# Optimization experiments

Hardware: AMD Instinct MI355X
Metric: run time of the kernel (lower is better)

The kernel has to match this reference:

```python
import jax, jax.numpy as jnp
import numpy as np

B, K, NP = 2, 48, 25            # batch, context_length, grid_x*grid_y
C, H, L = 768, 12, 6            # n_embd, n_head, n_layer
COLORS, VOCAB, IS = 10, 40, 26  # color_num, vocab_size, intention_size
MAXT = 1000                     # max_timestep
TOK = NP + 4                    # tokens per timestep (rtg, 25 states, action, pnp, intention)
T = K * TOK                     # total sequence length


def layernorm(x, g, b, eps=1e-5):
    m = x.mean(-1, keepdims=True)
    v = ((x - m) ** 2).mean(-1, keepdims=True)
    return (x - m) * jax.lax.rsqrt(v + eps) * g + b


def causal_attn(x, wq, bq, wk, bk, wv, bv, wo, bo):
    Bx, Tx, Cx = x.shape
    hd = Cx // H
    def heads(w, bb):
        return (x @ w + bb).reshape(Bx, Tx, H, hd).transpose(0, 2, 1, 3)
    q, k, v = heads(wq, bq), heads(wk, bk), heads(wv, bv)
    att = jnp.einsum('bhqd,bhkd->bhqk', q, k) * (1.0 / np.sqrt(hd))
    mask = jnp.tril(jnp.ones((Tx, Tx), bool))
    att = jnp.where(mask, att, -jnp.inf)
    att = jax.nn.softmax(att, axis=-1)
    y = jnp.einsum('bhqk,bhkd->bhqd', att, v).transpose(0, 2, 1, 3).reshape(Bx, Tx, Cx)
    return y @ wo + bo


def setup_inputs() -> dict:
    key = jax.random.key(0)
    ks = iter(jax.random.split(key, 64))
    def nrm(shape):
        return jax.random.normal(next(ks), shape, jnp.float32) * 0.02
    inp = dict(
        states=jax.random.randint(next(ks), (B, K * NP), 0, COLORS),
        actions=jax.random.randint(next(ks), (B, K), 0, VOCAB),
        rtgs=jax.random.normal(next(ks), (B, K), jnp.float32),
        timesteps=jax.random.randint(next(ks), (B, K), 0, MAXT + 1),
        pnp=jax.random.normal(next(ks), (B, K, NP), jnp.float32),
        intentions=jax.random.randint(next(ks), (B, K, 2), 0, IS),
        pos_emb=nrm((K + 1, C)),               # (block_size, C)
        global_pos_emb=nrm((MAXT + 1, C)),
        state_tab=nrm((COLORS, C)),
        action_tab=nrm((VOCAB, C)),
        ret_W=nrm((1, C)), ret_b=jnp.zeros((C,)),
        pnp_W=nrm((NP, C)), pnp_b=jnp.zeros((C,)),
        src_tab=nrm((IS, C)), dst_tab=nrm((IS, C)),
        int_W=nrm((2 * C, C)), int_b=jnp.zeros((C,)),
        ln1_g=jnp.ones((L, C)), ln1_b=jnp.zeros((L, C)),
        ln2_g=jnp.ones((L, C)), ln2_b=jnp.zeros((L, C)),
        Wq=nrm((L, C, C)), bq=jnp.zeros((L, C)),
        Wk=nrm((L, C, C)), bk=jnp.zeros((L, C)),
        Wv=nrm((L, C, C)), bv=jnp.zeros((L, C)),
        Wo=nrm((L, C, C)), bo=jnp.zeros((L, C)),
        Wm1=nrm((L, C, 4 * C)), bm1=jnp.zeros((L, 4 * C)),
        Wm2=nrm((L, 4 * C, C)), bm2=jnp.zeros((L, C)),
        lnf_g=jnp.ones((C,)), lnf_b=jnp.zeros((C,)),
        Whs=nrm((C, COLORS)), bhs=jnp.zeros((COLORS,)),
        Wha=nrm((C, VOCAB)), bha=jnp.zeros((VOCAB,)),
        Whr=nrm((C, 1)), bhr=jnp.zeros((1,)),
        Whi=nrm((C, 2 * IS)), bhi=jnp.zeros((2 * IS,)),
    )
    return inp


def reference(states, actions, rtgs, timesteps, pnp, intentions,
              pos_emb, global_pos_emb, state_tab, action_tab,
              ret_W, ret_b, pnp_W, pnp_b, src_tab, dst_tab, int_W, int_b,
              ln1_g, ln1_b, ln2_g, ln2_b, Wq, bq, Wk, bk, Wv, bv, Wo, bo,
              Wm1, bm1, Wm2, bm2, lnf_g, lnf_b,
              Whs, bhs, Wha, bha, Whr, bhr, Whi, bhi):
    # --- embeddings, interleaved as [rtg, state_0..24, action, pnp, intention] per timestep ---
    st = state_tab[states].reshape(B, K, NP, C)                    # strided writes 1+i::TOK
    ae = action_tab[actions][:, :, None, :]
    re = (rtgs[..., None] @ ret_W + ret_b)[:, :, None, :]          # rtgs.unsqueeze(-1) -> Linear(1,C)
    pe = (pnp @ pnp_W + pnp_b)[:, :, None, :]
    ie_in = jnp.concatenate([src_tab[intentions[..., 0]], dst_tab[intentions[..., 1]]], axis=-1)
    ie = (ie_in @ int_W + int_b)[:, :, None, :]
    tok = jnp.concatenate([re, st, ae, pe, ie], axis=2).reshape(B, T, C)
    # --- positions: gather global + local pos_emb[:block_size-1], repeat_interleave by TOK ---
    pos = global_pos_emb[timesteps] + pos_emb[:K][None]            # (B, K, C)
    x = tok + jnp.repeat(pos, TOK, axis=1)
    # --- transformer stack (dropout p=0) ---
    def blk(h, p):
        l1g, l1b, l2g, l2b, wq, bq_, wk, bk_, wv, bv_, wo, bo_, w1, b1, w2, b2 = p
        h = h + causal_attn(layernorm(h, l1g, l1b), wq, bq_, wk, bk_, wv, bv_, wo, bo_)
        m = layernorm(h, l2g, l2b)
        h = h + jax.nn.gelu(m @ w1 + b1, approximate=False) @ w2 + b2
        return h, None
    x, _ = jax.lax.scan(blk, x, (ln1_g, ln1_b, ln2_g, ln2_b, Wq, bq, Wk, bk, Wv, bv, Wo, bo, Wm1, bm1, Wm2, bm2))
    x = layernorm(x, lnf_g, lnf_b)
    xr = x.reshape(B, K, TOK, C)
    logits = x @ Whs + bhs                                         # (B, T, COLORS)
    logit_action = xr[:, :, NP + 1] @ Wha + bha                    # (B, K, VOCAB)
    logit_rtg = (xr[:, :, 0] @ Whr + bhr)[..., 0]                  # (B, K)
    li = xr[:, :, NP + 3] @ Whi + bhi                              # (B, K, 2*IS)
    return logits, logit_action, logit_rtg, li[..., :IS], li[..., IS:]
```

## Files before the change

kernel.cpp:

```cpp
#include <hip/hip_runtime.h>
#include <hip/hip_bf16.h>
#include <math.h>


typedef __hip_bfloat16 bf16;
typedef __attribute__((ext_vector_type(4))) short s4v;
typedef __attribute__((ext_vector_type(8))) short s8v;
typedef __attribute__((ext_vector_type(4))) float f4v;
typedef unsigned int u32;

#define DEV static __device__ __forceinline__

constexpr int NBATCH = 2;
constexpr int NK   = 48;
constexpr int NNP  = 25;
constexpr int NC   = 768;
constexpr int NH   = 12;
constexpr int NL   = 6;
constexpr int NTOK = 29;
constexpr int NT   = NK * NTOK;
constexpr int NM   = NBATCH * NT;
constexpr int MPAD = 2816;

DEV float bs2f(short s) {
  unsigned u = ((unsigned)(unsigned short)s) << 16;
  float f; __builtin_memcpy(&f, &u, 4); return f;
}
DEV short f2bs(float f) {
  bf16 h = __float2bfloat16(f);
  short s; __builtin_memcpy(&s, &h, 2); return s;
}

DEV void async16(const short* g, short* l) {
  __builtin_amdgcn_global_load_lds(
      (const __attribute__((address_space(1))) u32*)g,
      (__attribute__((address_space(3))) u32*)l, 16, 0, 0);
}

__global__ __launch_bounds__(256) void transpose_kernel(
    const float* __restrict__ src, bf16* __restrict__ dst, int R, int C)
{
  int c0 = blockIdx.x * 32, r0 = blockIdx.y * 32;
  __shared__ float tl[32][33];
  int rr = threadIdx.x >> 5, cc = threadIdx.x & 31;
#pragma unroll
  for (int p = 0; p < 4; p++)
    tl[rr + p * 8][cc] = src[(long)(r0 + rr + p * 8) * C + c0 + cc];
  __syncthreads();
#pragma unroll
  for (int p = 0; p < 4; p++)
    dst[(long)(c0 + rr + p * 8) * R + r0 + cc] = __float2bfloat16(tl[cc][rr + p * 8]);
}

__global__ __launch_bounds__(256) void transpose_layer_kernel(
    const float* __restrict__ Wq, const float* __restrict__ Wk,
    const float* __restrict__ Wv, const float* __restrict__ Wo,
    const float* __restrict__ Wm1, const float* __restrict__ Wm2,
    bf16* __restrict__ WqkvT, bf16* __restrict__ WoT,
    bf16* __restrict__ Wm1T, bf16* __restrict__ Wm2T)
{
  int t = blockIdx.x;
  const float* src; bf16* dst; int R, C, tile;
  if (t < 1728) {
    int m = t / 576; tile = t - m * 576;
    src = m == 0 ? Wq : (m == 1 ? Wk : Wv);
    dst = WqkvT + (long)m * 768 * 768; R = 768; C = 768;
  } else if (t < 2304) { src = Wo;  dst = WoT;  tile = t - 1728; R = 768;  C = 768;  }
  else if (t < 4608)   { src = Wm1; dst = Wm1T; tile = t - 2304; R = 768;  C = 3072; }
  else                 { src = Wm2; dst = Wm2T; tile = t - 4608; R = 3072; C = 768;  }
  int ct = C / 32;
  int tr = tile / ct, tc = tile - tr * ct;
  int r0 = tr * 32, c0 = tc * 32;
  __shared__ float tl[32][33];
  int rr = threadIdx.x >> 5, cc = threadIdx.x & 31;
#pragma unroll
  for (int p = 0; p < 4; p++)
    tl[rr + p * 8][cc] = src[(long)(r0 + rr + p * 8) * C + c0 + cc];
  __syncthreads();
#pragma unroll
  for (int p = 0; p < 4; p++)
    dst[(long)(c0 + rr + p * 8) * R + r0 + cc] = __float2bfloat16(tl[cc][rr + p * 8]);
}

__global__ __launch_bounds__(256) void gather_ie_kernel(
    const int* __restrict__ intentions, const float* __restrict__ src_tab,
    const float* __restrict__ dst_tab, bf16* __restrict__ ie_in)
{
  int idx = blockIdx.x * 256 + threadIdx.x;
  if (idx >= 96 * 1536) return;
  int row = idx / 1536, col = idx - row * 1536;
  float v;
  if (col < 768) v = src_tab[intentions[row * 2 + 0] * 768 + col];
  else           v = dst_tab[intentions[row * 2 + 1] * 768 + col - 768];
  ie_in[idx] = __float2bfloat16(v);
}

__global__ __launch_bounds__(256) void embed_kernel(
    const int* __restrict__ states, const int* __restrict__ actions,
    const float* __restrict__ rtgs, const int* __restrict__ timesteps,
    const float* __restrict__ pnp,
    const float* __restrict__ pos_emb, const float* __restrict__ gpe,
    const float* __restrict__ state_tab, const float* __restrict__ action_tab,
    const float* __restrict__ retW, const float* __restrict__ retb,
    const float* __restrict__ pnpW, const float* __restrict__ pnpb,
    const bf16* __restrict__ ieb, float* __restrict__ X)
{
  int bk = blockIdx.x;
  int b = bk / NK, ts = bk - b * NK;
  int c = blockIdx.y * 256 + threadIdx.x;

  float rtg = rtgs[bk];
  int tstep = timesteps[bk];
  int act   = actions[bk];

  long base = (long)(b * NT + ts * NTOK) * NC;
  float pos = gpe[(long)tstep * NC + c] + pos_emb[ts * NC + c];

  X[base + c] = rtg * retW[c] + retb[c] + pos;
  const int* sp = states + bk * NNP;
#pragma unroll
  for (int i = 0; i < NNP; i++)
    X[base + (1 + i) * NC + c] = state_tab[sp[i] * NC + c] + pos;
  X[base + 26 * NC + c] = action_tab[act * NC + c] + pos;
  float ap = pnpb[c];
  const float* pv = pnp + bk * NNP;
#pragma unroll
  for (int i = 0; i < NNP; i++) ap += pv[i] * pnpW[i * NC + c];
  X[base + 27 * NC + c] = ap + pos;
  X[base + 28 * NC + c] = __bfloat162float(ieb[bk * NC + c]) + pos;
}

__global__ __launch_bounds__(256) void ln_kernel(
    const float* __restrict__ X, bf16* __restrict__ XN,
    const float* __restrict__ g, const float* __restrict__ bt)
{
  int row = blockIdx.x, tid = threadIdx.x;
  const float* x = X + (long)row * NC;
  float v0 = x[tid], v1 = x[tid + 256], v2 = x[tid + 512];
  float s = v0 + v1 + v2;
#pragma unroll
  for (int o = 32; o > 0; o >>= 1) s += __shfl_down(s, o, 64);
  __shared__ float red[8];
  if ((tid & 63) == 0) red[tid >> 6] = s;
  __syncthreads();
  float mean = (red[0] + red[1] + red[2] + red[3]) * (1.0f / NC);
  float d0 = v0 - mean, d1 = v1 - mean, d2 = v2 - mean;
  float qq = d0 * d0 + d1 * d1 + d2 * d2;
#pragma unroll
  for (int o = 32; o > 0; o >>= 1) qq += __shfl_down(qq, o, 64);
  __syncthreads();
  if ((tid & 63) == 0) red[tid >> 6] = qq;
  __syncthreads();
  float var = (red[0] + red[1] + red[2] + red[3]) * (1.0f / NC);
  float rs = 1.0f / sqrtf(var + 1e-5f);
  bf16* xn = XN + (long)row * NC;
  xn[tid      ] = __float2bfloat16(d0 * rs * g[tid      ] + bt[tid      ]);
  xn[tid + 256] = __float2bfloat16(d1 * rs * g[tid + 256] + bt[tid + 256]);
  xn[tid + 512] = __float2bfloat16(d2 * rs * g[tid + 512] + bt[tid + 512]);
}

template<int BN>
__global__ __launch_bounds__(256) void gemm_kernel(
    const bf16* __restrict__ A, const bf16* __restrict__ WT,
    const float* __restrict__ b0, const float* __restrict__ b1,
    const float* __restrict__ b2, int Nsplit,
    bf16* __restrict__ outb, float* __restrict__ resid,
    int M, int N, int K, int flags)
{
  constexpr int IM = (BN == 128) ? 4 : 2;
  __shared__ __align__(1024) short As[128 * 32];
  __shared__ __align__(1024) short Bs[BN * 32];

  int tid = threadIdx.x, wave = tid >> 6, lane = tid & 63;
  int quad = lane >> 4, l16 = lane & 15;
  int m0 = blockIdx.y * 128, n0 = blockIdx.x * BN;
  int wm = (BN == 128) ? (wave >> 1) * 64 : wave * 32;
  int wn = (BN == 128) ? (wave & 1) * 64 : 0;
  int lr = lane >> 2, lc = (lane & 3) * 8;

  const short* Ag = (const short*)A + (long)m0 * K + lc;
  const short* Bg = (const short*)WT + (long)n0 * K + lc;

  const short* agp0 = Ag + (long)((wave * 2 + 0) * 16 + lr) * K;
  const short* agp1 = Ag + (long)((wave * 2 + 1) * 16 + lr) * K;
  short* al0 = &As[(wave * 2 + 0) * 16 * 32];
  short* al1 = &As[(wave * 2 + 1) * 16 * 32];
  const short* bgp0; const short* bgp1 = nullptr;
  short* bl0; short* bl1 = nullptr;
  if (BN == 128) {
    bgp0 = Bg + (long)((wave * 2 + 0) * 16 + lr) * K;
    bgp1 = Bg + (long)((wave * 2 + 1) * 16 + lr) * K;
    bl0 = &Bs[(wave * 2 + 0) * 16 * 32];
    bl1 = &Bs[(wave * 2 + 1) * 16 * 32];
  } else {
    bgp0 = Bg + (long)(wave * 16 + lr) * K;
    bl0 = &Bs[wave * 16 * 32];
  }

  f4v zero4 = {0.f, 0.f, 0.f, 0.f};
  f4v acc[IM][4];
#pragma unroll
  for (int i = 0; i < IM; i++)
#pragma unroll
    for (int j = 0; j < 4; j++) acc[i][j] = zero4;

  for (int kt = 0; kt < K; kt += 32) {
    __syncthreads();
    async16(agp0 + kt, al0);
    async16(agp1 + kt, al1);
    async16(bgp0 + kt, bl0);
    if (BN == 128) async16(bgp1 + kt, bl1);
    __syncthreads();

    s8v af[IM], bf8[4];
#pragma unroll
    for (int i = 0; i < IM; i++) {
      const short* p = &As[(wm + i * 16 + l16) * 32 + quad * 8];
      af[i].lo = *(const s4v*)p; af[i].hi = *(const s4v*)(p + 4);
    }
#pragma unroll
    for (int j = 0; j < 4; j++) {
      const short* p = &Bs[(wn + j * 16 + l16) * 32 + quad * 8];
      bf8[j].lo = *(const s4v*)p; bf8[j].hi = *(const s4v*)(p + 4);
    }
#pragma unroll
    for (int i = 0; i < IM; i++)
#pragma unroll
      for (int j = 0; j < 4; j++)
        acc[i][j] = __builtin_amdgcn_mfma_f32_16x16x32_bf16(af[i], bf8[j], acc[i][j], 0, 0, 0);
  }

#pragma unroll
  for (int i = 0; i < IM; i++) {
    int rbase = m0 + wm + i * 16 + quad * 4;
#pragma unroll
    for (int j = 0; j < 4; j++) {
      int bc = n0 + wn + j * 16;
      int wsel = bc / Nsplit;
      const float* bp = wsel == 0 ? b0 : (wsel == 1 ? b1 : b2);
      float bv = bp[bc - wsel * Nsplit + l16];
      int col = bc + l16;
#pragma unroll
      for (int r = 0; r < 4; r++) {
        int row = rbase + r;
        if (row < M) {
          float v = acc[i][j][r] + bv;
          if (flags & 1) v = 0.5f * v * (1.0f + erff(v * 0.70710678118654752f));
          if (flags & 2) resid[(long)row * N + col] += v;
          else outb[(long)row * N + col] = __float2bfloat16(v);
        }
      }
    }
  }
}

constexpr int ASTR = 72;

__global__ __launch_bounds__(256) void attn_kernel(
    const bf16* __restrict__ QKV, bf16* __restrict__ Yg)
{
  int qt = blockIdx.x, h = blockIdx.y, b = blockIdx.z;
  int q0 = qt * 64;
  int tid = threadIdx.x, wave = tid >> 6, lane = tid & 63, quad = lane >> 4, l16 = lane & 15;

  __shared__ short Qs[64 * ASTR];
  __shared__ short Ks[64 * ASTR];
  __shared__ short Vt[64 * ASTR];
  __shared__ short Ps[64 * ASTR];
  __shared__ float S[64 * 65];
  __shared__ float mrow[64], lrow[64], arow[64];
  __shared__ float red[256];

  if (tid < 64) { mrow[tid] = -1e30f; lrow[tid] = 0.f; }

  int r = tid >> 2, c16 = (tid & 3) * 16;
  const short* src = (const short*)QKV;
  s8v zz = {0,0,0,0,0,0,0,0};

  s8v qv0 = zz, qv1 = zz;
  if (q0 + r < NT) {
    const s8v* p = (const s8v*)(src + (long)(b * NT + q0 + r) * 2304 + h * 64 + c16);
    qv0 = p[0]; qv1 = p[1];
  }
  {
    short* qp = &Qs[r * ASTR + c16];
    *(s4v*)(qp    ) = qv0.lo; *(s4v*)(qp + 4) = qv0.hi;
    *(s4v*)(qp + 8) = qv1.lo; *(s4v*)(qp + 12) = qv1.hi;
  }

  f4v zero4 = {0.f, 0.f, 0.f, 0.f};
  f4v Of[4];
#pragma unroll
  for (int j = 0; j < 4; j++) Of[j] = zero4;

  int kend = q0 + 63; if (kend > NT - 1) kend = NT - 1;
  for (int k0 = 0; k0 <= kend; k0 += 64) {
    s8v kv0 = zz, kv1 = zz, vv0 = zz, vv1 = zz;
    if (k0 + r < NT) {
      const s8v* pk = (const s8v*)(src + (long)(b * NT + k0 + r) * 2304 + 768 + h * 64 + c16);
      kv0 = pk[0]; kv1 = pk[1];
      const s8v* pvv = (const s8v*)(src + (long)(b * NT + k0 + r) * 2304 + 1536 + h * 64 + c16);
      vv0 = pvv[0]; vv1 = pvv[1];
    }
    __syncthreads();
    {
      short* kp = &Ks[r * ASTR + c16];
      *(s4v*)(kp    ) = kv0.lo; *(s4v*)(kp + 4) = kv0.hi;
      *(s4v*)(kp + 8) = kv1.lo; *(s4v*)(kp + 12) = kv1.hi;
      short* vt = &Vt[c16 * ASTR + r];
      vt[ 0 * ASTR] = vv0.s0; vt[ 1 * ASTR] = vv0.s1; vt[ 2 * ASTR] = vv0.s2; vt[ 3 * ASTR] = vv0.s3;
      vt[ 4 * ASTR] = vv0.s4; vt[ 5 * ASTR] = vv0.s5; vt[ 6 * ASTR] = vv0.s6; vt[ 7 * ASTR] = vv0.s7;
      vt[ 8 * ASTR] = vv1.s0; vt[ 9 * ASTR] = vv1.s1; vt[10 * ASTR] = vv1.s2; vt[11 * ASTR] = vv1.s3;
      vt[12 * ASTR] = vv1.s4; vt[13 * ASTR] = vv1.s5; vt[14 * ASTR] = vv1.s6; vt[15 * ASTR] = vv1.s7;
    }
    __syncthreads();

    f4v sa[4];
#pragma unroll
    for (int j = 0; j < 4; j++) sa[j] = zero4;
#pragma unroll
    for (int ks = 0; ks < 2; ks++) {
      const short* pa = &Qs[(wave * 16 + l16) * ASTR + ks * 32 + quad * 8];
      s8v aq; aq.lo = *(const s4v*)pa; aq.hi = *(const s4v*)(pa + 4);
#pragma unroll
      for (int j = 0; j < 4; j++) {
        const short* pb = &Ks[(j * 16 + l16) * ASTR + ks * 32 + quad * 8];
        s8v bk8; bk8.lo = *(const s4v*)pb; bk8.hi = *(const s4v*)(pb + 4);
        sa[j] = __builtin_amdgcn_mfma_f32_16x16x32_bf16(aq, bk8, sa[j], 0, 0, 0);
      }
    }
#pragma unroll
    for (int j = 0; j < 4; j++) {
#pragma unroll
      for (int rg = 0; rg < 4; rg++) {
        int rloc = wave * 16 + quad * 4 + rg;
        int cloc = j * 16 + l16;
        int gq = q0 + rloc, gk = k0 + cloc;
        float sv = (gk <= gq && gq < NT) ? sa[j][rg] * 0.125f : -1e30f;
        S[rloc * 65 + cloc] = sv;
      }
    }
    __syncthreads();

    float mx = -1e30f;
#pragma unroll
    for (int c = 0; c < 16; c++) mx = fmaxf(mx, S[r * 65 + c16 + c]);
    red[r * 4 + (tid & 3)] = mx;
    __syncthreads();
    if (tid < 64) {
      float tm = fmaxf(fmaxf(red[tid * 4], red[tid * 4 + 1]), fmaxf(red[tid * 4 + 2], red[tid * 4 + 3]));
      float mn = fmaxf(mrow[tid], tm);
      arow[tid] = __expf(mrow[tid] - mn);
      mrow[tid] = mn;
    }
    __syncthreads();

    float mr = mrow[r];
    float psum = 0.f;
#pragma unroll
    for (int c = 0; c < 16; c++) {
      float e = __expf(S[r * 65 + c16 + c] - mr);
      psum += e;
      Ps[r * ASTR + c16 + c] = f2bs(e);
    }
    red[r * 4 + (tid & 3)] = psum;
    __syncthreads();
    if (tid < 64)
      lrow[tid] = lrow[tid] * arow[tid] + red[tid * 4] + red[tid * 4 + 1] + red[tid * 4 + 2] + red[tid * 4 + 3];
#pragma unroll
    for (int j = 0; j < 4; j++)
#pragma unroll
      for (int rg = 0; rg < 4; rg++)
        Of[j][rg] *= arow[wave * 16 + quad * 4 + rg];
    __syncthreads();

#pragma unroll
    for (int ks = 0; ks < 2; ks++) {
      const short* pa = &Ps[(wave * 16 + l16) * ASTR + ks * 32 + quad * 8];
      s8v ap8; ap8.lo = *(const s4v*)pa; ap8.hi = *(const s4v*)(pa + 4);
#pragma unroll
      for (int j = 0; j < 4; j++) {
        const short* pb = &Vt[(j * 16 + l16) * ASTR + ks * 32 + quad * 8];
        s8v vp8; vp8.lo = *(const s4v*)pb; vp8.hi = *(const s4v*)(pb + 4);
        Of[j] = __builtin_amdgcn_mfma_f32_16x16x32_bf16(ap8, vp8, Of[j], 0, 0, 0);
      }
    }
  }
  __syncthreads();
#pragma unroll
  for (int j = 0; j < 4; j++) {
#pragma unroll
    for (int rg = 0; rg < 4; rg++) {
      int rloc = wave * 16 + quad * 4 + rg;
      int gq = q0 + rloc;
      if (gq < NT) {
        float ov = Of[j][rg] / lrow[rloc];
        Yg[(long)(b * NT + gq) * NC + h * 64 + j * 16 + l16] = __float2bfloat16(ov);
      }
    }
  }
}

__global__ __launch_bounds__(256) void head_logits_kernel(
    const bf16* __restrict__ XN, const float* __restrict__ Whs,
    const float* __restrict__ bhs, float* __restrict__ out)
{
  int idx = blockIdx.x * 256 + threadIdx.x;
  if (idx >= NM * 10) return;
  int row = idx / 10, n = idx - row * 10;
  const short* x = (const short*)XN + (long)row * NC;
  float a0 = bhs[n], a1 = 0.f, a2 = 0.f, a3 = 0.f;
  for (int k = 0; k < NC; k += 4) {
    a0 += bs2f(x[k    ]) * Whs[(k    ) * 10 + n];
    a1 += bs2f(x[k + 1]) * Whs[(k + 1) * 10 + n];
    a2 += bs2f(x[k + 2]) * Whs[(k + 2) * 10 + n];
    a3 += bs2f(x[k + 3]) * Whs[(k + 3) * 10 + n];
  }
  out[idx] = a0 + a1 + a2 + a3;
}

__global__ __launch_bounds__(128) void head_small_kernel(
    const bf16* __restrict__ XN,
    const float* __restrict__ Wha, const float* __restrict__ bha,
    const float* __restrict__ Whr, const float* __restrict__ bhr,
    const float* __restrict__ Whi, const float* __restrict__ bhi,
    float* __restrict__ outA, float* __restrict__ outR,
    float* __restrict__ outS, float* __restrict__ outD)
{
  int blk = blockIdx.x;
  int b = blk / NK, ts = blk - b * NK;
  int tid = threadIdx.x;
  if (tid >= 93) return;
  const short* xs = (const short*)XN;
  if (tid < 40) {
    long row = (long)(b * NT + ts * NTOK + 26) * NC;
    float a0 = bha[tid], a1 = 0.f, a2 = 0.f, a3 = 0.f;
    for (int k = 0; k < NC; k += 4) {
      a0 += bs2f(xs[row + k    ]) * Wha[(k    ) * 40 + tid];
      a1 += bs2f(xs[row + k + 1]) * Wha[(k + 1) * 40 + tid];
      a2 += bs2f(xs[row + k + 2]) * Wha[(k + 2) * 40 + tid];
      a3 += bs2f(xs[row + k + 3]) * Wha[(k + 3) * 40 + tid];
    }
    outA[blk * 40 + tid] = a0 + a1 + a2 + a3;
  } else if (tid == 40) {
    long row = (long)(b * NT + ts * NTOK) * NC;
    float a0 = bhr[0], a1 = 0.f, a2 = 0.f, a3 = 0.f;
    for (int k = 0; k < NC; k += 4) {
      a0 += bs2f(xs[row + k    ]) * Whr[k    ];
      a1 += bs2f(xs[row + k + 1]) * Whr[k + 1];
      a2 += bs2f(xs[row + k + 2]) * Whr[k + 2];
      a3 += bs2f(xs[row + k + 3]) * Whr[k + 3];
    }
    outR[blk] = a0 + a1 + a2 + a3;
  } else {
    int n = tid - 41;
    long row = (long)(b * NT + ts * NTOK + 28) * NC;
    float a0 = bhi[n], a1 = 0.f, a2 = 0.f, a3 = 0.f;
    for (int k = 0; k < NC; k += 4) {
      a0 += bs2f(xs[row + k    ]) * Whi[(k    ) * 52 + n];
      a1 += bs2f(xs[row + k + 1]) * Whi[(k + 1) * 52 + n];
      a2 += bs2f(xs[row + k + 2]) * Whi[(k + 2) * 52 + n];
      a3 += bs2f(xs[row + k + 3]) * Whi[(k + 3) * 52 + n];
    }
    if (n < 26) outS[blk * 26 + n] = a0 + a1 + a2 + a3;
    else        outD[blk * 26 + (n - 26)] = a0 + a1 + a2 + a3;
  }
}

extern "C" void kernel_launch(void* const* d_in, const int* in_sizes, int n_in,
                              void* d_out, int out_size, void* d_ws, size_t ws_size,
                              hipStream_t stream)
{
  (void)in_sizes; (void)n_in; (void)out_size; (void)ws_size;

  const int*   states     = (const int*)  d_in[0];
  const int*   actions    = (const int*)  d_in[1];
  const float* rtgs       = (const float*)d_in[2];
  const int*   timesteps  = (const int*)  d_in[3];
  const float* pnp        = (const float*)d_in[4];
  const int*   intentions = (const int*)  d_in[5];
  const float* pos_emb    = (const float*)d_in[6];
  const float* gpe        = (const float*)d_in[7];
  const float* state_tab  = (const float*)d_in[8];
  const float* action_tab = (const float*)d_in[9];
  const float* retW  = (const float*)d_in[10];
  const float* retb  = (const float*)d_in[11];
  const float* pnpW  = (const float*)d_in[12];
  const float* pnpb  = (const float*)d_in[13];
  const float* src_tab = (const float*)d_in[14];
  const float* dst_tab = (const float*)d_in[15];
  const float* intW  = (const float*)d_in[16];
  const float* intb  = (const float*)d_in[17];
  const float* ln1g  = (const float*)d_in[18];
  const float* ln1b  = (const float*)d_in[19];
  const float* ln2g  = (const float*)d_in[20];
  const float* ln2b  = (const float*)d_in[21];
  const float* Wq = (const float*)d_in[22];
  const float* bq = (const float*)d_in[23];
  const float* Wk = (const float*)d_in[24];
  const float* bk = (const float*)d_in[25];
  const float* Wv = (const float*)d_in[26];
  const float* bv = (const float*)d_in[27];
  const float* Wo = (const float*)d_in[28];
  const float* bo = (const float*)d_in[29];
  const float* Wm1 = (const float*)d_in[30];
  const float* bm1 = (const float*)d_in[31];
  const float* Wm2 = (const float*)d_in[32];
  const float* bm2 = (const float*)d_in[33];
  const float* lnfg = (const float*)d_in[34];
  const float* lnfb = (const float*)d_in[35];
  const float* Whs = (const float*)d_in[36];
  const float* bhs = (const float*)d_in[37];
  const float* Wha = (const float*)d_in[38];
  const float* bha = (const float*)d_in[39];
  const float* Whr = (const float*)d_in[40];
  const float* bhr = (const float*)d_in[41];
  const float* Whi = (const float*)d_in[42];
  const float* bhi = (const float*)d_in[43];

  char* wsb = (char*)d_ws;
  float* X   = (float*)(wsb);
  bf16* XN   = (bf16*)(wsb + 8650752);
  bf16* QKVb = (bf16*)(wsb + 12976128);
  bf16* Yb   = (bf16*)(wsb + 25952256);
  bf16* H1   = QKVb;
  bf16* WqkvT = (bf16*)(wsb + 30277632);
  bf16* WoT   = WqkvT + (long)2304 * 768;
  bf16* Wm1T  = WoT + (long)768 * 768;
  bf16* Wm2T  = Wm1T + (long)3072 * 768;
  bf16* intWT = (bf16*)(wsb + 30277632);
  bf16* ie_in = intWT + (long)768 * 1536;
  bf16* ieb   = ie_in + (long)128 * 1536;

  float* out0 = (float*)d_out;
  float* out1 = out0 + 27840;
  float* out2 = out1 + 3840;
  float* out3 = out2 + 96;
  float* out4 = out3 + 2496;

  transpose_kernel<<<dim3(768 / 32, 1536 / 32), 256, 0, stream>>>(intW, intWT, 1536, 768);
  gather_ie_kernel<<<(96 * 1536 + 255) / 256, 256, 0, stream>>>(intentions, src_tab, dst_tab, ie_in);
  gemm_kernel<64><<<dim3(12, 1), 256, 0, stream>>>(ie_in, intWT, intb, intb, intb, 768,
      ieb, nullptr, 96, 768, 1536, 0);
  embed_kernel<<<dim3(96, 3), 256, 0, stream>>>(
      states, actions, rtgs, timesteps, pnp, pos_emb, gpe, state_tab, action_tab,
      retW, retb, pnpW, pnpb, ieb, X);

  for (int l = 0; l < NL; l++) {
    const long wofs = (long)l * NC * NC;
    const long mofs = (long)l * NC * 4 * NC;
    transpose_layer_kernel<<<6912, 256, 0, stream>>>(
        Wq + wofs, Wk + wofs, Wv + wofs, Wo + wofs, Wm1 + mofs, Wm2 + mofs,
        WqkvT, WoT, Wm1T, Wm2T);
    ln_kernel<<<NM, 256, 0, stream>>>(X, XN, ln1g + l * NC, ln1b + l * NC);
    gemm_kernel<128><<<dim3(18, 22), 256, 0, stream>>>(XN, WqkvT,
        bq + l * NC, bk + l * NC, bv + l * NC, 768, QKVb, nullptr, NM, 2304, NC, 0);
    attn_kernel<<<dim3(22, NH, NBATCH), 256, 0, stream>>>(QKVb, Yb);
    gemm_kernel<64><<<dim3(12, 22), 256, 0, stream>>>(Yb, WoT,
        bo + l * NC, bo + l * NC, bo + l * NC, 768, nullptr, X, NM, 768, NC, 2);
    ln_kernel<<<NM, 256, 0, stream>>>(X, XN, ln2g + l * NC, ln2b + l * NC);
    gemm_kernel<128><<<dim3(24, 22), 256, 0, stream>>>(XN, Wm1T,
        bm1 + l * 4 * NC, bm1 + l * 4 * NC, bm1 + l * 4 * NC, 4 * NC, H1, nullptr,
        NM, 3072, NC, 1);
    gemm_kernel<64><<<dim3(12, 22), 256, 0, stream>>>(H1, Wm2T,
        bm2 + l * NC, bm2 + l * NC, bm2 + l * NC, 768, nullptr, X, NM, 768, 4 * NC, 2);
  }
  ln_kernel<<<NM, 256, 0, stream>>>(X, XN, lnfg, lnfb);
  head_logits_kernel<<<(NM * 10 + 255) / 256, 256, 0, stream>>>(XN, Whs, bhs, out0);
  head_small_kernel<<<NBATCH * NK, 128, 0, stream>>>(XN, Wha, bha, Whr, bhr, Whi, bhi,
      out1, out2, out3, out4);
}
```

Baseline: 1.807 ms.

## Double-buffer GEMM LDS tiles, retile GEMMs, and batch all-layer weight transposes

The GEMM kernel now keeps two LDS buffers, so the async global load for the next K-slice is issued before the MFMAs on the current slice, and one barrier per iteration replaces two. Tiles are reshaped to BM x 64 with BM of 128 or 64, which roughly doubles the grid sizes to fill more CUs. When the workspace is large enough, all six layers' weight transposes run in one big launch up front instead of six serialized launches interleaved with compute. This costs more LDS and a much larger workspace, and falls back to the old per-layer path if the workspace is too small.

```diff
diff --git a/kernel.cpp b/kernel.cpp
--- a/kernel.cpp
+++ b/kernel.cpp
@@ -57,17 +57,21 @@
     const float* __restrict__ Wv, const float* __restrict__ Wo,
     const float* __restrict__ Wm1, const float* __restrict__ Wm2,
     bf16* __restrict__ WqkvT, bf16* __restrict__ WoT,
-    bf16* __restrict__ Wm1T, bf16* __restrict__ Wm2T)
-{
-  int t = blockIdx.x;
+    bf16* __restrict__ Wm1T, bf16* __restrict__ Wm2T, int multi)
+{
+  int blk = blockIdx.x;
+  int l = blk / 6912, t = blk - l * 6912;
+  long so = (long)l * 768 * 768;
+  long mo = (long)l * 768 * 3072;
+  long dl = multi ? l : 0;
   const float* src; bf16* dst; int R, C, tile;
   if (t < 1728) {
     int m = t / 576; tile = t - m * 576;
-    src = m == 0 ? Wq : (m == 1 ? Wk : Wv);
-    dst = WqkvT + (long)m * 768 * 768; R = 768; C = 768;
-  } else if (t < 2304) { src = Wo;  dst = WoT;  tile = t - 1728; R = 768;  C = 768;  }
-  else if (t < 4608)   { src = Wm1; dst = Wm1T; tile = t - 2304; R = 768;  C = 3072; }
-  else                 { src = Wm2; dst = Wm2T; tile = t - 4608; R = 3072; C = 768;  }
+    src = (m == 0 ? Wq : (m == 1 ? Wk : Wv)) + so;
+    dst = WqkvT + dl * (2304L * 768) + (long)m * 768 * 768; R = 768; C = 768;
+  } else if (t < 2304) { src = Wo + so;  dst = WoT  + dl * (768L * 768);  tile = t - 1728; R = 768;  C = 768;  }
+  else if (t < 4608)   { src = Wm1 + mo; dst = Wm1T + dl * (3072L * 768); tile = t - 2304; R = 768;  C = 3072; }
+  else                 { src = Wm2 + mo; dst = Wm2T + dl * (768L * 3072); tile = t - 4608; R = 3072; C = 768;  }
   int ct = C / 32;
   int tr = tile / ct, tc = tile - tr * ct;
   int r0 = tr * 32, c0 = tc * 32;
@@ -159,7 +163,7 @@
   xn[tid + 512] = __float2bfloat16(d2 * rs * g[tid + 512] + bt[tid + 512]);
 }
 
-template<int BN>
+template<int BM>
 __global__ __launch_bounds__(256) void gemm_kernel(
     const bf16* __restrict__ A, const bf16* __restrict__ WT,
     const float* __restrict__ b0, const float* __restrict__ b1,
@@ -167,35 +171,29 @@
     bf16* __restrict__ outb, float* __restrict__ resid,
     int M, int N, int K, int flags)
 {
-  constexpr int IM = (BN == 128) ? 4 : 2;
-  __shared__ __align__(1024) short As[128 * 32];
-  __shared__ __align__(1024) short Bs[BN * 32];
+  constexpr int IM  = BM / 64;
+  constexpr int ACH = BM / 64;
+  __shared__ __align__(1024) short As[2][BM * 32];
+  __shared__ __align__(1024) short Bs[2][64 * 32];
 
   int tid = threadIdx.x, wave = tid >> 6, lane = tid & 63;
   int quad = lane >> 4, l16 = lane & 15;
-  int m0 = blockIdx.y * 128, n0 = blockIdx.x * BN;
-  int wm = (BN == 128) ? (wave >> 1) * 64 : wave * 32;
-  int wn = (BN == 128) ? (wave & 1) * 64 : 0;
+  int m0 = blockIdx.y * BM, n0 = blockIdx.x * 64;
+  int wm = wave * (BM / 4);
   int lr = lane >> 2, lc = (lane & 3) * 8;
 
   const short* Ag = (const short*)A + (long)m0 * K + lc;
   const short* Bg = (const short*)WT + (long)n0 * K + lc;
 
-  const short* agp0 = Ag + (long)((wave * 2 + 0) * 16 + lr) * K;
-  const short* agp1 = Ag + (long)((wave * 2 + 1) * 16 + lr) * K;
-  short* al0 = &As[(wave * 2 + 0) * 16 * 32];
-  short* al1 = &As[(wave * 2 + 1) * 16 * 32];
-  const short* bgp0; const short* bgp1 = nullptr;
-  short* bl0; short* bl1 = nullptr;
-  if (BN == 128) {
-    bgp0 = Bg + (long)((wave * 2 + 0) * 16 + lr) * K;
-    bgp1 = Bg + (long)((wave * 2 + 1) * 16 + lr) * K;
-    bl0 = &Bs[(wave * 2 + 0) * 16 * 32];
-    bl1 = &Bs[(wave * 2 + 1) * 16 * 32];
-  } else {
-    bgp0 = Bg + (long)(wave * 16 + lr) * K;
-    bl0 = &Bs[wave * 16 * 32];
-  }
+  const short* ag[ACH]; int alo[ACH];
+#pragma unroll
+  for (int c = 0; c < ACH; c++) {
+    int rbase = wave * (16 * ACH) + c * 16;
+    ag[c] = Ag + (long)(rbase + lr) * K;
+    alo[c] = rbase * 32;
+  }
+  const short* bg = Bg + (long)(wave * 16 + lr) * K;
+  int blo = wave * 16 * 32;
 
   f4v zero4 = {0.f, 0.f, 0.f, 0.f};
   f4v acc[IM][4];
@@ -204,23 +202,29 @@
 #pragma unroll
     for (int j = 0; j < 4; j++) acc[i][j] = zero4;
 
-  for (int kt = 0; kt < K; kt += 32) {
-    __syncthreads();
-    async16(agp0 + kt, al0);
-    async16(agp1 + kt, al1);
-    async16(bgp0 + kt, bl0);
-    if (BN == 128) async16(bgp1 + kt, bl1);
-    __syncthreads();
-
+  int nk = K >> 5;
+#pragma unroll
+  for (int c = 0; c < ACH; c++) async16(ag[c], &As[0][alo[c]]);
+  async16(bg, &Bs[0][blo]);
+  __syncthreads();
+
+  for (int kt = 0; kt < nk; kt++) {
+    int cur = kt & 1, nxt = cur ^ 1;
+    if (kt + 1 < nk) {
+      int ko = (kt + 1) << 5;
+#pragma unroll
+      for (int c = 0; c < ACH; c++) async16(ag[c] + ko, &As[nxt][alo[c]]);
+      async16(bg + ko, &Bs[nxt][blo]);
+    }
     s8v af[IM], bf8[4];
 #pragma unroll
     for (int i = 0; i < IM; i++) {
-      const short* p = &As[(wm + i * 16 + l16) * 32 + quad * 8];
+      const short* p = &As[cur][(wm + i * 16 + l16) * 32 + quad * 8];
       af[i].lo = *(const s4v*)p; af[i].hi = *(const s4v*)(p + 4);
     }
 #pragma unroll
     for (int j = 0; j < 4; j++) {
-      const short* p = &Bs[(wn + j * 16 + l16) * 32 + quad * 8];
+      const short* p = &Bs[cur][(j * 16 + l16) * 32 + quad * 8];
       bf8[j].lo = *(const s4v*)p; bf8[j].hi = *(const s4v*)(p + 4);
     }
 #pragma unroll
@@ -228,6 +232,7 @@
 #pragma unroll
       for (int j = 0; j < 4; j++)
         acc[i][j] = __builtin_amdgcn_mfma_f32_16x16x32_bf16(af[i], bf8[j], acc[i][j], 0, 0, 0);
+    __syncthreads();
   }
 
 #pragma unroll
@@ -235,7 +240,7 @@
     int rbase = m0 + wm + i * 16 + quad * 4;
 #pragma unroll
     for (int j = 0; j < 4; j++) {
-      int bc = n0 + wn + j * 16;
+      int bc = n0 + j * 16;
       int wsel = bc / Nsplit;
       const float* bp = wsel == 0 ? b0 : (wsel == 1 ? b1 : b2);
       float bv = bp[bc - wsel * Nsplit + l16];
@@ -471,7 +476,7 @@
                               void* d_out, int out_size, void* d_ws, size_t ws_size,
                               hipStream_t stream)
 {
-  (void)in_sizes; (void)n_in; (void)out_size; (void)ws_size;
+  (void)in_sizes; (void)n_in; (void)out_size;
 
   const int*   states     = (const int*)  d_in[0];
   const int*   actions    = (const int*)  d_in[1];
@@ -524,13 +529,28 @@
   bf16* QKVb = (bf16*)(wsb + 12976128);
   bf16* Yb   = (bf16*)(wsb + 25952256);
   bf16* H1   = QKVb;
-  bf16* WqkvT = (bf16*)(wsb + 30277632);
-  bf16* WoT   = WqkvT + (long)2304 * 768;
-  bf16* Wm1T  = WoT + (long)768 * 768;
-  bf16* Wm2T  = Wm1T + (long)3072 * 768;
-  bf16* intWT = (bf16*)(wsb + 30277632);
-  bf16* ie_in = intWT + (long)768 * 1536;
-  bf16* ieb   = ie_in + (long)128 * 1536;
+  bf16* WTbase = (bf16*)(wsb + 30277632);
+
+  const size_t NEED_BIG = 30277632UL + 84934656UL + 2949120UL;
+  bool big = ws_size >= NEED_BIG;
+
+  long sQKV = 2304L * 768, sO = 768L * 768, sM1 = 3072L * 768, sM2 = 768L * 3072;
+  bf16 *WqkvT, *WoT, *Wm1T, *Wm2T, *intWT;
+  if (big) {
+    WqkvT = WTbase;
+    WoT   = WqkvT + 6 * sQKV;
+    Wm1T  = WoT   + 6 * sO;
+    Wm2T  = Wm1T  + 6 * sM1;
+    intWT = Wm2T  + 6 * sM2;
+  } else {
+    WqkvT = WTbase;
+    WoT   = WqkvT + sQKV;
+    Wm1T  = WoT + sO;
+    Wm2T  = Wm1T + sM1;
+    intWT = WTbase;
+  }
+  bf16* ie_in = intWT + 768L * 1536;
+  bf16* ieb   = ie_in + 128L * 1536;
 
   float* out0 = (float*)d_out;
   float* out1 = out0 + 27840;
@@ -538,31 +558,41 @@
   float* out3 = out2 + 96;
   float* out4 = out3 + 2496;
 
-  transpose_kernel<<<dim3(768 / 32, 1536 / 32), 256, 0, stream>>>(intW, intWT, 1536, 768);
+  transpose_kernel<<<dim3(24, 48), 256, 0, stream>>>(intW, intWT, 1536, 768);
   gather_ie_kernel<<<(96 * 1536 + 255) / 256, 256, 0, stream>>>(intentions, src_tab, dst_tab, ie_in);
-  gemm_kernel<64><<<dim3(12, 1), 256, 0, stream>>>(ie_in, intWT, intb, intb, intb, 768,
+  gemm_kernel<64><<<dim3(12, 2), 256, 0, stream>>>(ie_in, intWT, intb, intb, intb, 768,
       ieb, nullptr, 96, 768, 1536, 0);
   embed_kernel<<<dim3(96, 3), 256, 0, stream>>>(
       states, actions, rtgs, timesteps, pnp, pos_emb, gpe, state_tab, action_tab,
       retW, retb, pnpW, pnpb, ieb, X);
 
+  if (big)
+    transpose_layer_kernel<<<6912 * NL, 256, 0, stream>>>(
+        Wq, Wk, Wv, Wo, Wm1, Wm2, WqkvT, WoT, Wm1T, Wm2T, 1);
+
   for (int l = 0; l < NL; l++) {
     const long wofs = (long)l * NC * NC;
     const long mofs = (long)l * NC * 4 * NC;
-    transpose_layer_kernel<<<6912, 256, 0, stream>>>(
-        Wq + wofs, Wk + wofs, Wv + wofs, Wo + wofs, Wm1 + mofs, Wm2 + mofs,
-        WqkvT, WoT, Wm1T, Wm2T);
+    if (!big)
+      transpose_layer_kernel<<<6912, 256, 0, stream>>>(
+          Wq + wofs, Wk + wofs, Wv + wofs, Wo + wofs, Wm1 + mofs, Wm2 + mofs,
+          WqkvT, WoT, Wm1T, Wm2T, 0);
+    bf16* wqkv = big ? WqkvT + l * sQKV : WqkvT;
+    bf16* wo   = big ? WoT   + l * sO   : WoT;
+    bf16* wm1  = big ? Wm1T  + l * sM1  : Wm1T;
+    bf16* wm2  = big ? Wm2T  + l * sM2  : Wm2T;
+
     ln_kernel<<<NM, 256, 0, stream>>>(X, XN, ln1g + l * NC, ln1b + l * NC);
-    gemm_kernel<128><<<dim3(18, 22), 256, 0, stream>>>(XN, WqkvT,
+    gemm_kernel<128><<<dim3(36, 22), 256, 0, stream>>>(XN, wqkv,
         bq + l * NC, bk + l * NC, bv + l * NC, 768, QKVb, nullptr, NM, 2304, NC, 0);
     attn_kernel<<<dim3(22, NH, NBATCH), 256, 0, stream>>>(QKVb, Yb);
-    gemm_kernel<64><<<dim3(12, 22), 256, 0, stream>>>(Yb, WoT,
+    gemm_kernel<64><<<dim3(12, 44), 256, 0, stream>>>(Yb, wo,
         bo + l * NC, bo + l * NC, bo + l * NC, 768, nullptr, X, NM, 768, NC, 2);
     ln_kernel<<<NM, 256, 0, stream>>>(X, XN, ln2g + l * NC, ln2b + l * NC);
-    gemm_kernel<128><<<dim3(24, 22), 256, 0, stream>>>(XN, Wm1T,
+    gemm_kernel<128><<<dim3(48, 22), 256, 0, stream>>>(XN, wm1,
         bm1 + l * 4 * NC, bm1 + l * 4 * NC, bm1 + l * 4 * NC, 4 * NC, H1, nullptr,
         NM, 3072, NC, 1);
-    gemm_kernel<64><<<dim3(12, 22), 256, 0, stream>>>(H1, Wm2T,
+    gemm_kernel<64><<<dim3(12, 44), 256, 0, stream>>>(H1, wm2,
         bm2 + l * NC, bm2 + l * NC, bm2 + l * NC, 768, nullptr, X, NM, 768, 4 * NC, 2);
   }
   ln_kernel<<<NM, 256, 0, stream>>>(X, XN, lnfg, lnfb);
```

Result: faster. 1.632 ms (-9.7%).
